# Kernel tuning notes

Measured on AMD Instinct MI355X. Metric: run time of the kernel, lower is better.

Reference implementation:

```python
import jax, jax.numpy as jnp
import numpy as np


def setup_inputs() -> dict:
    key = jax.random.key(0)
    k1, k2 = jax.random.split(key)
    b, feat = 8192, 256
    x = jax.random.normal(k1, (b, feat), dtype=jnp.float32)
    y = jax.random.randint(k2, (b,), 0, 100, dtype=jnp.int64)
    T = jnp.zeros((1,), dtype=jnp.float32)
    return {"x": x, "y": y, "T": T}


def reference(x, y, T):
    # SNNLoss.forward with inv=False, d=None, and no -1 labels in y
    b = x.shape[0]
    x = x / jnp.std(x, ddof=1)  # torch .std() is unbiased (ddof=1)

    # Pairwise Euclidean distance via Gram matrix (avoids [b,b,feat] blowup)
    sq = jnp.sum(x * x, axis=1)  # [b]
    d2 = jnp.maximum(sq[:, None] + sq[None, :] - 2.0 * (x @ x.T), 0.0)  # [b,b]
    eye = jnp.eye(b, dtype=bool)
    # diagonal is exactly 0 and masked out later; keep sqrt grad-safe there
    dist = jnp.where(eye, 0.0, jnp.sqrt(jnp.where(eye, 1.0, d2)))

    e_dist = -dist * jnp.power(jnp.float32(10.0), T[0])  # [b,b]
    neg_inf = jnp.float32(-jnp.inf)

    # denominator: all pairs except self
    den_dist = jnp.where(eye, neg_inf, e_dist)
    den = jax.scipy.special.logsumexp(den_dist, axis=1)  # [b]

    # numerator: same-label pairs except self
    m_num = (y[:, None] == y[None, :]) & ~eye  # [b,b]
    has = jnp.any(m_num, axis=1)  # rows with at least one positive
    num_dist = jnp.where(m_num, e_dist, neg_inf)
    # rows with no positives would give logsumexp = -inf; torch code zeroes
    # both num and den there. Substitute finite values, then zero the term.
    num = jax.scipy.special.logsumexp(jnp.where(has[:, None], num_dist, 0.0), axis=1)
    terms = jnp.where(has, num - den, 0.0)
    return -jnp.mean(terms)
```

## Files before the change

### kernel.cpp

```cpp
#include <hip/hip_runtime.h>

#define B_ROWS 8192
#define FEAT   256
#define NCH    4
#define CH_COLS 2048
#define NJT    16

typedef float f32x4 __attribute__((ext_vector_type(4)));
typedef _Float16 f16x8 __attribute__((ext_vector_type(8)));

typedef const __attribute__((address_space(1))) unsigned int* gas_ptr;
typedef __attribute__((address_space(3))) unsigned int* las_ptr;

__device__ __forceinline__ void gload_lds16(const void* g, void* l) {
  __builtin_amdgcn_global_load_lds((gas_ptr)g, (las_ptr)l, 16, 0, 0);
}

__global__ __launch_bounds__(256) void prep_kernel(
    const float* __restrict__ x, unsigned short* __restrict__ xh,
    float* __restrict__ sq, float* __restrict__ part_s,
    float* __restrict__ part_q)
{
  int tid = threadIdx.x;
  int l = tid & 63, wid = tid >> 6;
  int row = blockIdx.x * 4 + wid;
  const float4* xv = (const float4*)(x + (size_t)row * FEAT);
  float4 v = xv[l];
  ushort4 u;
  u.x = __builtin_bit_cast(unsigned short, (_Float16)v.x);
  u.y = __builtin_bit_cast(unsigned short, (_Float16)v.y);
  u.z = __builtin_bit_cast(unsigned short, (_Float16)v.z);
  u.w = __builtin_bit_cast(unsigned short, (_Float16)v.w);
  ((ushort4*)(xh + (size_t)row * FEAT))[l] = u;
  float ssq  = v.x*v.x + v.y*v.y + v.z*v.z + v.w*v.w;
  float ssum = v.x + v.y + v.z + v.w;
  #pragma unroll
  for (int m = 32; m; m >>= 1) {
    ssq  += __shfl_xor(ssq, m);
    ssum += __shfl_xor(ssum, m);
  }
  if (l == 0) sq[row] = ssq;
  __shared__ float red[8];
  if (l == 0) { red[wid*2] = ssum; red[wid*2+1] = ssq; }
  __syncthreads();
  if (tid == 0) {
    part_s[blockIdx.x] = red[0]+red[2]+red[4]+red[6];
    part_q[blockIdx.x] = red[1]+red[3]+red[5]+red[7];
  }
}

__global__ __launch_bounds__(256) void reduce_kernel(
    const float* __restrict__ part_s, const float* __restrict__ part_q,
    double* __restrict__ gacc)
{
  int tid = threadIdx.x;
  double s = 0.0, q = 0.0;
  #pragma unroll
  for (int k = 0; k < 8; ++k) {
    s += (double)part_s[tid + 256*k];
    q += (double)part_q[tid + 256*k];
  }
  #pragma unroll
  for (int m = 32; m; m >>= 1) {
    s += __shfl_xor(s, m);
    q += __shfl_xor(q, m);
  }
  __shared__ double rs[4], rq[4];
  if ((tid & 63) == 0) { rs[tid >> 6] = s; rq[tid >> 6] = q; }
  __syncthreads();
  if (tid == 0) {
    gacc[0] = rs[0]+rs[1]+rs[2]+rs[3];
    gacc[1] = rq[0]+rq[1]+rq[2]+rq[3];
  }
}

template<bool DIAG>
__device__ __forceinline__ void epilogue(
    const f32x4 (&acc)[2][4], const float* __restrict__ sq,
    const int* __restrict__ y, int j0, int wc, int l15,
    int i0q, const float (&sqi)[8], const int (&yiv)[8],
    float (&sden)[8], float (&snum)[8], float nscale2)
{
  int jb = j0 + wc*64 + l15;
  float sqj[4]; int yj[4];
  #pragma unroll
  for (int cb = 0; cb < 4; ++cb) {
    int j = jb + cb*16;
    sqj[cb] = sq[j];
    yj[cb]  = y[j];
  }
  #pragma unroll
  for (int rb = 0; rb < 2; ++rb) {
    #pragma unroll
    for (int r = 0; r < 4; ++r) {
      float si = sqi[rb*4+r];
      int   ig = i0q + rb*16 + r;
      int   yi = yiv[rb*4+r];
      float dacc = 0.f, nacc = 0.f;
      #pragma unroll
      for (int cb = 0; cb < 4; ++cb) {
        float S  = acc[rb][cb][r];
        float d2 = fmaf(S, -2.0f, si + sqj[cb]);
        d2 = fmaxf(d2, 0.0f);
        float e  = __builtin_amdgcn_exp2f(__builtin_amdgcn_sqrtf(d2) * nscale2);
        bool offd = !DIAG || (ig != jb + cb*16);
        dacc += offd ? e : 0.0f;
        nacc += (yi == yj[cb] && offd) ? e : 0.0f;
      }
      sden[rb*4+r] += dacc;
      snum[rb*4+r] += nacc;
    }
  }
}

__global__ __launch_bounds__(512, 2) void snn_main(
    const unsigned short* __restrict__ xh, const float* __restrict__ sq,
    const int* __restrict__ y, const float* __restrict__ T,
    const double* __restrict__ gacc,
    float* __restrict__ pden, float* __restrict__ pnum)
{
  extern __shared__ char smem[];
  char* lA = smem;
  char* lB = smem + 65536;
  int tid = threadIdx.x;
  int l = tid & 63, wid = tid >> 6;
  int wr = wid >> 1, wc = wid & 1;
  int quad = l >> 4, l15 = l & 15;
  int l5 = l >> 5, s31 = l & 31;
  int ch = blockIdx.x, it = blockIdx.y;
  int i0 = it * 128, chbase = ch * CH_COLS;

  const char* xbc = (const char*)xh;

  {
    const char* gA = xbc + (size_t)i0 * 512;
    #pragma unroll
    for (int s = 0; s < 8; ++s) {
      int c  = wid*8 + s;
      int rw = 2*c + l5;
      int gg = s31 ^ (rw & 7);
      gload_lds16(gA + rw*512 + gg*16, lA + c*1024);
    }
  }

  double ssum = gacc[0], sssq = gacc[1];
  const double n = (double)B_ROWS * FEAT;
  double var = (sssq - ssum * ssum / n) / (n - 1.0);
  float stdv = (float)sqrt(var);
  float p10  = __builtin_amdgcn_exp2f(T[0] * 3.3219280948873623f);
  float nscale2 = -(p10 * 1.4426950408889634f / stdv);

  int dj = -1;
  if (i0 >= chbase && i0 < chbase + CH_COLS) dj = (i0 - chbase) >> 7;

  float sqi[8]; int yiv[8];
  int i0q = i0 + wr*32 + quad*4;
  #pragma unroll
  for (int rb = 0; rb < 2; ++rb)
    #pragma unroll
    for (int r = 0; r < 4; ++r) {
      int idx = i0q + rb*16 + r;
      sqi[rb*4+r] = sq[idx];
      yiv[rb*4+r] = y[idx];
    }

  float sden[8], snum[8];
  #pragma unroll
  for (int v = 0; v < 8; ++v) { sden[v] = 0.f; snum[v] = 0.f; }
  f32x4 acc[2][4];
  const f32x4 zero4 = {0.f, 0.f, 0.f, 0.f};

  for (int jt = 0; jt < NJT; ++jt) {
    int j0 = chbase + jt * 128;

    __syncthreads();
    {
      const char* gB = xbc + (size_t)j0 * 512;
      #pragma unroll
      for (int s = 0; s < 8; ++s) {
        int c  = wid*8 + s;
        int rw = 2*c + l5;
        int gg = s31 ^ (rw & 7);
        gload_lds16(gB + rw*512 + gg*16, lB + c*1024);
      }
    }

    if (jt > 0) {
      int pj0 = j0 - 128;
      if (jt - 1 == dj)
        epilogue<true >(acc, sq, y, pj0, wc, l15, i0q, sqi, yiv, sden, snum, nscale2);
      else
        epilogue<false>(acc, sq, y, pj0, wc, l15, i0q, sqi, yiv, sden, snum, nscale2);
    }
    #pragma unroll
    for (int rb = 0; rb < 2; ++rb)
      #pragma unroll
      for (int cb = 0; cb < 4; ++cb)
        acc[rb][cb] = zero4;

    __syncthreads();

    #pragma unroll
    for (int kk = 0; kk < 8; ++kk) {
      f16x8 av[2], bv[4];
      #pragma unroll
      for (int rb = 0; rb < 2; ++rb) {
        int rw = wr*32 + rb*16 + l15;
        av[rb] = *(const f16x8*)(lA + rw*512 + ((((kk<<2)|quad) ^ (l15 & 7)) << 4));
      }
      #pragma unroll
      for (int cb = 0; cb < 4; ++cb) {
        int rw = wc*64 + cb*16 + l15;
        bv[cb] = *(const f16x8*)(lB + rw*512 + ((((kk<<2)|quad) ^ (l15 & 7)) << 4));
      }
      #pragma unroll
      for (int rb = 0; rb < 2; ++rb)
        #pragma unroll
        for (int cb = 0; cb < 4; ++cb)
          acc[rb][cb] = __builtin_amdgcn_mfma_f32_16x16x32_f16(av[rb], bv[cb], acc[rb][cb], 0, 0, 0);
    }
  }
  {
    int pj0 = chbase + (NJT-1) * 128;
    if (NJT-1 == dj)
      epilogue<true >(acc, sq, y, pj0, wc, l15, i0q, sqi, yiv, sden, snum, nscale2);
    else
      epilogue<false>(acc, sq, y, pj0, wc, l15, i0q, sqi, yiv, sden, snum, nscale2);
  }

  #pragma unroll
  for (int v = 0; v < 8; ++v) {
    #pragma unroll
    for (int m = 1; m <= 8; m <<= 1) {
      sden[v] += __shfl_xor(sden[v], m);
      snum[v] += __shfl_xor(snum[v], m);
    }
  }
  if (l15 == 0) {
    int base = ((it*NCH + ch)*2 + wc) * 128;
    #pragma unroll
    for (int rb = 0; rb < 2; ++rb)
      #pragma unroll
      for (int r = 0; r < 4; ++r) {
        int rin = wr*32 + rb*16 + quad*4 + r;
        pden[base + rin] = sden[rb*4+r];
        pnum[base + rin] = snum[rb*4+r];
      }
  }
}

__global__ __launch_bounds__(256) void final_kernel(
    const float* __restrict__ pden, const float* __restrict__ pnum,
    float* __restrict__ out)
{
  int row = blockIdx.x*256 + threadIdx.x;
  int itt = row >> 7, rin = row & 127;
  float den = 0.f, num = 0.f;
  #pragma unroll
  for (int p = 0; p < 8; ++p) {
    den += pden[(itt*8 + p)*128 + rin];
    num += pnum[(itt*8 + p)*128 + rin];
  }
  float t = (num > 0.f)
          ? 0.6931471805599453f *
            (__builtin_amdgcn_logf(num) - __builtin_amdgcn_logf(den)) : 0.f;
  #pragma unroll
  for (int m = 32; m; m >>= 1) t += __shfl_xor(t, m);
  __shared__ float red[4];
  if ((threadIdx.x & 63) == 0) red[threadIdx.x >> 6] = t;
  __syncthreads();
  if (threadIdx.x == 0)
    atomicAdd(out, -(red[0]+red[1]+red[2]+red[3]) * (1.0f/8192.0f));
}

extern "C" void kernel_launch(void* const* d_in, const int* in_sizes, int n_in,
                              void* d_out, int out_size, void* d_ws, size_t ws_size,
                              hipStream_t stream)
{
  (void)in_sizes; (void)n_in; (void)out_size; (void)ws_size;
  const float* x  = (const float*)d_in[0];
  const int* y    = (const int*)d_in[1];
  const float* T  = (const float*)d_in[2];
  char* ws = (char*)d_ws;
  double* gacc  = (double*)ws;
  float* part_s = (float*)(ws + 1024);
  float* part_q = (float*)(ws + 1024 + 8192);
  float* sq     = (float*)(ws + 32768);
  unsigned short* xh = (unsigned short*)(ws + 65536);
  float* pden   = (float*)(ws + 65536 + 4194304);
  float* pnum   = pden + 64*8*128;

  hipMemsetAsync(d_out, 0, sizeof(float), stream);
  hipLaunchKernelGGL(prep_kernel, dim3(B_ROWS/4), dim3(256), 0, stream,
                     x, xh, sq, part_s, part_q);
  hipLaunchKernelGGL(reduce_kernel, dim3(1), dim3(256), 0, stream,
                     part_s, part_q, gacc);
  hipFuncSetAttribute((const void*)snn_main,
                      hipFuncAttributeMaxDynamicSharedMemorySize, 131072);
  hipLaunchKernelGGL(snn_main, dim3(NCH, B_ROWS/128), dim3(512), 131072, stream,
                     xh, sq, y, T, gacc, pden, pnum);
  hipLaunchKernelGGL(final_kernel, dim3(32), dim3(256), 0, stream,
                     pden, pnum, (float*)d_out);
}
```

Before: 128.8 us.

## Keep A tile in registers, shrink B tiles, fold reductions into main kernel

The A row-tile now lives in registers loaded straight from global memory instead of LDS, and the B tile shrinks to 64 columns in a 32KB static LDS buffer. Blocks drop to 256 threads and the grid doubles to 8 column chunks. The std reduction kernel and the memset are removed: every block re-reduces the partial sums itself, and the final kernel becomes a single block that writes the output directly. This cuts launches and LDS use so more blocks can be resident, at the cost of higher register pressure and redundant partial-sum reads in every block.

```diff
diff --git a/kernel.cpp b/kernel.cpp
--- a/kernel.cpp
+++ b/kernel.cpp
@@ -2,8 +2,8 @@
 
 #define B_ROWS 8192
 #define FEAT   256
-#define NCH    4
-#define CH_COLS 2048
+#define NCH    8
+#define CH_COLS 1024
 #define NJT    16
 
 typedef float f32x4 __attribute__((ext_vector_type(4)));
@@ -49,39 +49,14 @@
   }
 }
 
-__global__ __launch_bounds__(256) void reduce_kernel(
-    const float* __restrict__ part_s, const float* __restrict__ part_q,
-    double* __restrict__ gacc)
-{
-  int tid = threadIdx.x;
-  double s = 0.0, q = 0.0;
-  #pragma unroll
-  for (int k = 0; k < 8; ++k) {
-    s += (double)part_s[tid + 256*k];
-    q += (double)part_q[tid + 256*k];
-  }
-  #pragma unroll
-  for (int m = 32; m; m >>= 1) {
-    s += __shfl_xor(s, m);
-    q += __shfl_xor(q, m);
-  }
-  __shared__ double rs[4], rq[4];
-  if ((tid & 63) == 0) { rs[tid >> 6] = s; rq[tid >> 6] = q; }
-  __syncthreads();
-  if (tid == 0) {
-    gacc[0] = rs[0]+rs[1]+rs[2]+rs[3];
-    gacc[1] = rq[0]+rq[1]+rq[2]+rq[3];
-  }
-}
-
 template<bool DIAG>
 __device__ __forceinline__ void epilogue(
     const f32x4 (&acc)[2][4], const float* __restrict__ sq,
-    const int* __restrict__ y, int j0, int wc, int l15,
+    const int* __restrict__ y, int j0, int l15,
     int i0q, const float (&sqi)[8], const int (&yiv)[8],
     float (&sden)[8], float (&snum)[8], float nscale2)
 {
-  int jb = j0 + wc*64 + l15;
+  int jb = j0 + l15;
   float sqj[4]; int yj[4];
   #pragma unroll
   for (int cb = 0; cb < 4; ++cb) {
@@ -113,48 +88,48 @@
   }
 }
 
-__global__ __launch_bounds__(512, 2) void snn_main(
+__global__ __launch_bounds__(256, 2) void snn_main(
     const unsigned short* __restrict__ xh, const float* __restrict__ sq,
     const int* __restrict__ y, const float* __restrict__ T,
-    const double* __restrict__ gacc,
+    const float* __restrict__ part_s, const float* __restrict__ part_q,
     float* __restrict__ pden, float* __restrict__ pnum)
 {
-  extern __shared__ char smem[];
-  char* lA = smem;
-  char* lB = smem + 65536;
+  __shared__ __align__(16) char lB[32768];
   int tid = threadIdx.x;
   int l = tid & 63, wid = tid >> 6;
-  int wr = wid >> 1, wc = wid & 1;
   int quad = l >> 4, l15 = l & 15;
   int l5 = l >> 5, s31 = l & 31;
   int ch = blockIdx.x, it = blockIdx.y;
   int i0 = it * 128, chbase = ch * CH_COLS;
-
   const char* xbc = (const char*)xh;
 
-  {
-    const char* gA = xbc + (size_t)i0 * 512;
-    #pragma unroll
-    for (int s = 0; s < 8; ++s) {
-      int c  = wid*8 + s;
-      int rw = 2*c + l5;
-      int gg = s31 ^ (rw & 7);
-      gload_lds16(gA + rw*512 + gg*16, lA + c*1024);
-    }
-  }
-
-  double ssum = gacc[0], sssq = gacc[1];
+  f16x8 areg[2][8];
+  #pragma unroll
+  for (int rb = 0; rb < 2; ++rb)
+    #pragma unroll
+    for (int kk = 0; kk < 8; ++kk)
+      areg[rb][kk] = *(const f16x8*)(xbc +
+          (size_t)(i0 + wid*32 + rb*16 + l15)*512 + kk*64 + quad*16);
+
+  float s_acc = 0.f, q_acc = 0.f;
+  #pragma unroll
+  for (int t = 0; t < 32; ++t) {
+    s_acc += part_s[l + 64*t];
+    q_acc += part_q[l + 64*t];
+  }
+  #pragma unroll
+  for (int m = 1; m <= 32; m <<= 1) {
+    s_acc += __shfl_xor(s_acc, m);
+    q_acc += __shfl_xor(q_acc, m);
+  }
   const double n = (double)B_ROWS * FEAT;
-  double var = (sssq - ssum * ssum / n) / (n - 1.0);
+  double var = ((double)q_acc - (double)s_acc*(double)s_acc/n) / (n - 1.0);
   float stdv = (float)sqrt(var);
   float p10  = __builtin_amdgcn_exp2f(T[0] * 3.3219280948873623f);
   float nscale2 = -(p10 * 1.4426950408889634f / stdv);
 
-  int dj = -1;
-  if (i0 >= chbase && i0 < chbase + CH_COLS) dj = (i0 - chbase) >> 7;
-
   float sqi[8]; int yiv[8];
-  int i0q = i0 + wr*32 + quad*4;
+  int i0q = i0 + wid*32 + quad*4;
   #pragma unroll
   for (int rb = 0; rb < 2; ++rb)
     #pragma unroll
@@ -171,7 +146,7 @@
   const f32x4 zero4 = {0.f, 0.f, 0.f, 0.f};
 
   for (int jt = 0; jt < NJT; ++jt) {
-    int j0 = chbase + jt * 128;
+    int j0 = chbase + jt * 64;
 
     __syncthreads();
     {
@@ -186,11 +161,11 @@
     }
 
     if (jt > 0) {
-      int pj0 = j0 - 128;
-      if (jt - 1 == dj)
-        epilogue<true >(acc, sq, y, pj0, wc, l15, i0q, sqi, yiv, sden, snum, nscale2);
+      int pj0 = j0 - 64;
+      if (pj0 == i0 || pj0 == i0 + 64)
+        epilogue<true >(acc, sq, y, pj0, l15, i0q, sqi, yiv, sden, snum, nscale2);
       else
-        epilogue<false>(acc, sq, y, pj0, wc, l15, i0q, sqi, yiv, sden, snum, nscale2);
+        epilogue<false>(acc, sq, y, pj0, l15, i0q, sqi, yiv, sden, snum, nscale2);
     }
     #pragma unroll
     for (int rb = 0; rb < 2; ++rb)
@@ -202,30 +177,25 @@
 
     #pragma unroll
     for (int kk = 0; kk < 8; ++kk) {
-      f16x8 av[2], bv[4];
-      #pragma unroll
-      for (int rb = 0; rb < 2; ++rb) {
-        int rw = wr*32 + rb*16 + l15;
-        av[rb] = *(const f16x8*)(lA + rw*512 + ((((kk<<2)|quad) ^ (l15 & 7)) << 4));
-      }
+      f16x8 bv[4];
       #pragma unroll
       for (int cb = 0; cb < 4; ++cb) {
-        int rw = wc*64 + cb*16 + l15;
-        bv[cb] = *(const f16x8*)(lB + rw*512 + ((((kk<<2)|quad) ^ (l15 & 7)) << 4));
+        int nr = cb*16 + l15;
+        bv[cb] = *(const f16x8*)(lB + nr*512 + ((((kk<<2)|quad) ^ (l15 & 7)) << 4));
       }
       #pragma unroll
       for (int rb = 0; rb < 2; ++rb)
         #pragma unroll
         for (int cb = 0; cb < 4; ++cb)
-          acc[rb][cb] = __builtin_amdgcn_mfma_f32_16x16x32_f16(av[rb], bv[cb], acc[rb][cb], 0, 0, 0);
+          acc[rb][cb] = __builtin_amdgcn_mfma_f32_16x16x32_f16(areg[rb][kk], bv[cb], acc[rb][cb], 0, 0, 0);
     }
   }
   {
-    int pj0 = chbase + (NJT-1) * 128;
-    if (NJT-1 == dj)
-      epilogue<true >(acc, sq, y, pj0, wc, l15, i0q, sqi, yiv, sden, snum, nscale2);
+    int pj0 = chbase + (NJT-1) * 64;
+    if (pj0 == i0 || pj0 == i0 + 64)
+      epilogue<true >(acc, sq, y, pj0, l15, i0q, sqi, yiv, sden, snum, nscale2);
     else
-      epilogue<false>(acc, sq, y, pj0, wc, l15, i0q, sqi, yiv, sden, snum, nscale2);
+      epilogue<false>(acc, sq, y, pj0, l15, i0q, sqi, yiv, sden, snum, nscale2);
   }
 
   #pragma unroll
@@ -237,40 +207,49 @@
     }
   }
   if (l15 == 0) {
-    int base = ((it*NCH + ch)*2 + wc) * 128;
+    int base = (it*NCH + ch) * 128;
     #pragma unroll
     for (int rb = 0; rb < 2; ++rb)
       #pragma unroll
       for (int r = 0; r < 4; ++r) {
-        int rin = wr*32 + rb*16 + quad*4 + r;
+        int rin = wid*32 + rb*16 + quad*4 + r;
         pden[base + rin] = sden[rb*4+r];
         pnum[base + rin] = snum[rb*4+r];
       }
   }
 }
 
-__global__ __launch_bounds__(256) void final_kernel(
+__global__ __launch_bounds__(1024) void final_kernel(
     const float* __restrict__ pden, const float* __restrict__ pnum,
     float* __restrict__ out)
 {
-  int row = blockIdx.x*256 + threadIdx.x;
-  int itt = row >> 7, rin = row & 127;
-  float den = 0.f, num = 0.f;
-  #pragma unroll
-  for (int p = 0; p < 8; ++p) {
-    den += pden[(itt*8 + p)*128 + rin];
-    num += pnum[(itt*8 + p)*128 + rin];
-  }
-  float t = (num > 0.f)
-          ? 0.6931471805599453f *
-            (__builtin_amdgcn_logf(num) - __builtin_amdgcn_logf(den)) : 0.f;
-  #pragma unroll
-  for (int m = 32; m; m >>= 1) t += __shfl_xor(t, m);
-  __shared__ float red[4];
-  if ((threadIdx.x & 63) == 0) red[threadIdx.x >> 6] = t;
+  int tid = threadIdx.x;
+  float tot = 0.f;
+  #pragma unroll
+  for (int rr = 0; rr < 8; ++rr) {
+    int row = tid + 1024*rr;
+    int itt = row >> 7, rin = row & 127;
+    float den = 0.f, num = 0.f;
+    #pragma unroll
+    for (int p = 0; p < NCH; ++p) {
+      den += pden[(itt*NCH + p)*128 + rin];
+      num += pnum[(itt*NCH + p)*128 + rin];
+    }
+    if (num > 0.f)
+      tot += 0.6931471805599453f *
+             (__builtin_amdgcn_logf(num) - __builtin_amdgcn_logf(den));
+  }
+  #pragma unroll
+  for (int m = 32; m; m >>= 1) tot += __shfl_xor(tot, m);
+  __shared__ float red[16];
+  if ((tid & 63) == 0) red[tid >> 6] = tot;
   __syncthreads();
-  if (threadIdx.x == 0)
-    atomicAdd(out, -(red[0]+red[1]+red[2]+red[3]) * (1.0f/8192.0f));
+  if (tid == 0) {
+    float s = 0.f;
+    #pragma unroll
+    for (int w = 0; w < 16; ++w) s += red[w];
+    out[0] = -s / 8192.0f;
+  }
 }
 
 extern "C" void kernel_launch(void* const* d_in, const int* in_sizes, int n_in,
@@ -282,23 +261,17 @@
   const int* y    = (const int*)d_in[1];
   const float* T  = (const float*)d_in[2];
   char* ws = (char*)d_ws;
-  double* gacc  = (double*)ws;
   float* part_s = (float*)(ws + 1024);
   float* part_q = (float*)(ws + 1024 + 8192);
   float* sq     = (float*)(ws + 32768);
   unsigned short* xh = (unsigned short*)(ws + 65536);
   float* pden   = (float*)(ws + 65536 + 4194304);
-  float* pnum   = pden + 64*8*128;
-
-  hipMemsetAsync(d_out, 0, sizeof(float), stream);
+  float* pnum   = pden + 64*NCH*128;
+
   hipLaunchKernelGGL(prep_kernel, dim3(B_ROWS/4), dim3(256), 0, stream,
                      x, xh, sq, part_s, part_q);
-  hipLaunchKernelGGL(reduce_kernel, dim3(1), dim3(256), 0, stream,
-                     part_s, part_q, gacc);
-  hipFuncSetAttribute((const void*)snn_main,
-                      hipFuncAttributeMaxDynamicSharedMemorySize, 131072);
-  hipLaunchKernelGGL(snn_main, dim3(NCH, B_ROWS/128), dim3(512), 131072, stream,
-                     xh, sq, y, T, gacc, pden, pnum);
-  hipLaunchKernelGGL(final_kernel, dim3(32), dim3(256), 0, stream,
+  hipLaunchKernelGGL(snn_main, dim3(NCH, B_ROWS/128), dim3(256), 0, stream,
+                     xh, sq, y, T, part_s, part_q, pden, pnum);
+  hipLaunchKernelGGL(final_kernel, dim3(1), dim3(1024), 0, stream,
                      pden, pnum, (float*)d_out);
 }
```

New measurement: 120.8 us. 6.2% less time.
